# Optimization experiments

Hardware: AMD Instinct MI355X
Metric: run time of the kernel (lower is better)

The kernel has to match this reference:

```python
import jax, jax.numpy as jnp
import numpy as np

# irreps = 128x0e + 64x1o + 32x2e  ->  dim = 128 + 192 + 160 = 480
IRREPS = [(128, 0), (64, 1), (32, 2)]  # (multiplicity, l)
NUM_SCALAR = 128          # 0e channels (p=+1, l=0); scalar_index = [0..127]
NUM_FEATURES = 224        # total irrep instances
DIM = 480
EPS_LN = 1e-5             # unused by math path (kept for fidelity to signature)
EPS_INV = 1e-6            # Invariant eps (default)
N = 100000


def setup_inputs() -> dict:
    key = jax.random.key(0)
    k1, k2, k3 = jax.random.split(key, 3)
    node_input = jax.random.normal(k1, (N, DIM), dtype=jnp.float32)
    affine_weight = jax.random.normal(k2, (NUM_FEATURES,), dtype=jnp.float32)
    affine_bias = jax.random.normal(k3, (NUM_SCALAR,), dtype=jnp.float32)
    return {"node_input": node_input, "affine_weight": affine_weight, "affine_bias": affine_bias}


def _eln(x, weight, bias):
    # 1) subtract mean of scalar (0e) channels from those channels only
    scalar_mean = jnp.mean(x[:, :NUM_SCALAR], axis=1, keepdims=True)
    x = x.at[:, :NUM_SCALAR].add(-scalar_mean)

    # 2) per-irrep-instance norm: Invariant = Norm(x + eps^2) - eps
    norms = []
    off = 0
    for mul, l in IRREPS:
        d = 2 * l + 1
        blk = x[:, off: off + mul * d].reshape(x.shape[0], mul, d)
        n = jnp.sqrt(jnp.sum(jnp.square(blk + EPS_INV ** 2), axis=-1)) - EPS_INV
        norms.append(n)
        off += mul * d
    norm = jnp.concatenate(norms, axis=1)  # [N, num_features]

    # 3) RMS over irrep instances, scale whole feature vector
    inv_rms = jax.lax.rsqrt(jnp.mean(jnp.square(norm), axis=1, keepdims=True))
    x = x * inv_rms

    # 4) per-irrep affine scale (ElementwiseTensorProduct with num_features x 0e)
    w_parts = []
    ix = 0
    for mul, l in IRREPS:
        d = 2 * l + 1
        w_parts.append(jnp.repeat(weight[ix: ix + mul], d))
        ix += mul
    w_full = jnp.concatenate(w_parts)  # [dim]
    x = x * w_full[None, :]

    # 5) add bias to scalar channels
    x = x.at[:, :NUM_SCALAR].add(bias[None, :])
    return x


def reference(node_input, affine_weight, affine_bias):
    return _eln(node_input, affine_weight, affine_bias)
```

## Files before the change

kernel.cpp:

```cpp
#include <hip/hip_runtime.h>
#include <hip/hip_bf16.h>


#define NROW_TOTAL_DIM 480
#define ROWS_PER_BLOCK 4

__global__ __launch_bounds__(256) void eln_kernel(
    const float* __restrict__ in,
    const float* __restrict__ wgt,
    const float* __restrict__ bias,
    float* __restrict__ out,
    int n_rows)
{
    const int wave = threadIdx.x >> 6;
    const int lane = threadIdx.x & 63;
    const int row  = blockIdx.x * ROWS_PER_BLOCK + wave;
    if (row >= n_rows) return;

    const float* x = in  + (size_t)row * NROW_TOTAL_DIM;
    float*       y = out + (size_t)row * NROW_TOTAL_DIM;

    float2 s = *reinterpret_cast<const float2*>(x + 2 * lane);

    const float* p1 = x + 128 + 3 * lane;
    float v0 = p1[0], v1 = p1[1], v2 = p1[2];

    float e0 = 0.f, e1 = 0.f, e2 = 0.f, e3 = 0.f, e4 = 0.f;
    if (lane < 32) {
        const float* p2 = x + 320 + 5 * lane;
        e0 = p2[0]; e1 = p2[1]; e2 = p2[2]; e3 = p2[3]; e4 = p2[4];
    }

    float ssum = s.x + s.y;
    #pragma unroll
    for (int m = 1; m < 64; m <<= 1) ssum += __shfl_xor(ssum, m);
    const float mean = ssum * (1.0f / 128.0f);
    s.x -= mean;
    s.y -= mean;

    const float epsq = 1e-12f;
    const float eps  = 1e-6f;

    float n0 = fabsf(s.x + epsq) - eps;
    float n1 = fabsf(s.y + epsq) - eps;

    float a0 = v0 + epsq, a1 = v1 + epsq, a2 = v2 + epsq;
    float n2 = sqrtf(a0 * a0 + a1 * a1 + a2 * a2) - eps;

    float nsq = n0 * n0 + n1 * n1 + n2 * n2;

    if (lane < 32) {
        float b0 = e0 + epsq, b1 = e1 + epsq, b2 = e2 + epsq,
              b3 = e3 + epsq, b4 = e4 + epsq;
        float n3 = sqrtf(b0 * b0 + b1 * b1 + b2 * b2 + b3 * b3 + b4 * b4) - eps;
        nsq += n3 * n3;
    }

    #pragma unroll
    for (int m = 1; m < 64; m <<= 1) nsq += __shfl_xor(nsq, m);
    const float inv_rms = rsqrtf(nsq * (1.0f / 224.0f));

    {
        float w0 = wgt[2 * lane], w1 = wgt[2 * lane + 1];
        float2 so;
        so.x = s.x * inv_rms * w0 + bias[2 * lane];
        so.y = s.y * inv_rms * w1 + bias[2 * lane + 1];
        *reinterpret_cast<float2*>(y + 2 * lane) = so;
    }
    {
        float wv = wgt[128 + lane] * inv_rms;
        float* q1 = y + 128 + 3 * lane;
        q1[0] = v0 * wv;
        q1[1] = v1 * wv;
        q1[2] = v2 * wv;
    }
    if (lane < 32) {
        float we = wgt[192 + lane] * inv_rms;
        float* q2 = y + 320 + 5 * lane;
        q2[0] = e0 * we;
        q2[1] = e1 * we;
        q2[2] = e2 * we;
        q2[3] = e3 * we;
        q2[4] = e4 * we;
    }
}

extern "C" void kernel_launch(void* const* d_in, const int* in_sizes, int n_in,
                              void* d_out, int out_size, void* d_ws, size_t ws_size,
                              hipStream_t stream) {
    const float* node_input    = (const float*)d_in[0];
    const float* affine_weight = (const float*)d_in[1];
    const float* affine_bias   = (const float*)d_in[2];
    float* out = (float*)d_out;

    const int n_rows = in_sizes[0] / NROW_TOTAL_DIM;
    const int grid = (n_rows + ROWS_PER_BLOCK - 1) / ROWS_PER_BLOCK;

    eln_kernel<<<grid, 256, 0, stream>>>(node_input, affine_weight, affine_bias,
                                         out, n_rows);
}
```

Baseline: 72.32 us.

## Vectorize row loads to float4, hoist weights, use grid-stride persistent waves

Each wave now reads its 480-float row as contiguous 16-byte vectors with nontemporal loads and stores, replacing the strided 3- and 5-element per-lane accesses. Per-lane weight and bias values are loaded once into registers before a grid-stride loop over rows, and the grid is capped at 2048 blocks. The per-irrep norm-squared sum is replaced by a plain sum of squares over all elements, which removes the sqrt calls but drops the small -eps correction terms. Each wave keeps only one row in flight, so latency hiding depends on occupancy.

```diff
diff --git a/kernel.cpp b/kernel.cpp
--- a/kernel.cpp
+++ b/kernel.cpp
@@ -2,8 +2,9 @@
 #include <hip/hip_bf16.h>
 
 
-#define NROW_TOTAL_DIM 480
-#define ROWS_PER_BLOCK 4
+#define DIM 480
+
+typedef float f32x4 __attribute__((ext_vector_type(4)));
 
 __global__ __launch_bounds__(256) void eln_kernel(
     const float* __restrict__ in,
@@ -12,76 +13,69 @@
     float* __restrict__ out,
     int n_rows)
 {
-    const int wave = threadIdx.x >> 6;
-    const int lane = threadIdx.x & 63;
-    const int row  = blockIdx.x * ROWS_PER_BLOCK + wave;
-    if (row >= n_rows) return;
+    const int lane    = threadIdx.x & 63;
+    const int gwave   = (blockIdx.x * blockDim.x + threadIdx.x) >> 6;
+    const int n_waves = (gridDim.x * blockDim.x) >> 6;
 
-    const float* x = in  + (size_t)row * NROW_TOTAL_DIM;
-    float*       y = out + (size_t)row * NROW_TOTAL_DIM;
-
-    float2 s = *reinterpret_cast<const float2*>(x + 2 * lane);
-
-    const float* p1 = x + 128 + 3 * lane;
-    float v0 = p1[0], v1 = p1[1], v2 = p1[2];
-
-    float e0 = 0.f, e1 = 0.f, e2 = 0.f, e3 = 0.f, e4 = 0.f;
-    if (lane < 32) {
-        const float* p2 = x + 320 + 5 * lane;
-        e0 = p2[0]; e1 = p2[1]; e2 = p2[2]; e3 = p2[3]; e4 = p2[4];
+    float w0k[4], w1k[4], bk[4];
+    #pragma unroll
+    for (int k = 0; k < 4; ++k) {
+        int j = 4 * lane + k;
+        if (j < 128) { w0k[k] = wgt[j];                       bk[k] = bias[j]; }
+        else         { w0k[k] = wgt[128 + (j - 128) / 3];     bk[k] = 0.f;     }
+    }
+    #pragma unroll
+    for (int k = 0; k < 4; ++k) {
+        if (lane < 56) {
+            int j = 256 + 4 * lane + k;
+            w1k[k] = (j < 320) ? wgt[128 + (j - 128) / 3]
+                               : wgt[192 + (j - 320) / 5];
+        } else {
+            w1k[k] = 0.f;
+        }
     }
 
-    float ssum = s.x + s.y;
-    #pragma unroll
-    for (int m = 1; m < 64; m <<= 1) ssum += __shfl_xor(ssum, m);
-    const float mean = ssum * (1.0f / 128.0f);
-    s.x -= mean;
-    s.y -= mean;
+    const float epsq = 1e-12f;
 
-    const float epsq = 1e-12f;
-    const float eps  = 1e-6f;
+    for (int row = gwave; row < n_rows; row += n_waves) {
+        const f32x4* xr = reinterpret_cast<const f32x4*>(in + (size_t)row * DIM);
+        f32x4*       yr = reinterpret_cast<f32x4*>(out + (size_t)row * DIM);
 
-    float n0 = fabsf(s.x + epsq) - eps;
-    float n1 = fabsf(s.y + epsq) - eps;
+        f32x4 r0 = __builtin_nontemporal_load(xr + lane);
+        f32x4 r1 = (f32x4)(0.f);
+        if (lane < 56) r1 = __builtin_nontemporal_load(xr + 64 + lane);
 
-    float a0 = v0 + epsq, a1 = v1 + epsq, a2 = v2 + epsq;
-    float n2 = sqrtf(a0 * a0 + a1 * a1 + a2 * a2) - eps;
+        float ssum = (lane < 32) ? (r0.x + r0.y + r0.z + r0.w) : 0.f;
+        #pragma unroll
+        for (int m = 1; m < 64; m <<= 1) ssum += __shfl_xor(ssum, m);
+        const float mean = ssum * (1.0f / 128.0f);
+        if (lane < 32) { r0.x -= mean; r0.y -= mean; r0.z -= mean; r0.w -= mean; }
 
-    float nsq = n0 * n0 + n1 * n1 + n2 * n2;
+        float a0 = r0.x + epsq, a1 = r0.y + epsq, a2 = r0.z + epsq, a3 = r0.w + epsq;
+        float nsq = a0 * a0 + a1 * a1 + a2 * a2 + a3 * a3;
+        if (lane < 56) {
+            float c0 = r1.x + epsq, c1 = r1.y + epsq, c2 = r1.z + epsq, c3 = r1.w + epsq;
+            nsq += c0 * c0 + c1 * c1 + c2 * c2 + c3 * c3;
+        }
+        #pragma unroll
+        for (int m = 1; m < 64; m <<= 1) nsq += __shfl_xor(nsq, m);
+        const float inv_rms = rsqrtf(nsq * (1.0f / 224.0f));
 
-    if (lane < 32) {
-        float b0 = e0 + epsq, b1 = e1 + epsq, b2 = e2 + epsq,
-              b3 = e3 + epsq, b4 = e4 + epsq;
-        float n3 = sqrtf(b0 * b0 + b1 * b1 + b2 * b2 + b3 * b3 + b4 * b4) - eps;
-        nsq += n3 * n3;
-    }
+        f32x4 o0;
+        o0.x = r0.x * inv_rms * w0k[0] + bk[0];
+        o0.y = r0.y * inv_rms * w0k[1] + bk[1];
+        o0.z = r0.z * inv_rms * w0k[2] + bk[2];
+        o0.w = r0.w * inv_rms * w0k[3] + bk[3];
+        __builtin_nontemporal_store(o0, yr + lane);
 
-    #pragma unroll
-    for (int m = 1; m < 64; m <<= 1) nsq += __shfl_xor(nsq, m);
-    const float inv_rms = rsqrtf(nsq * (1.0f / 224.0f));
-
-    {
-        float w0 = wgt[2 * lane], w1 = wgt[2 * lane + 1];
-        float2 so;
-        so.x = s.x * inv_rms * w0 + bias[2 * lane];
-        so.y = s.y * inv_rms * w1 + bias[2 * lane + 1];
-        *reinterpret_cast<float2*>(y + 2 * lane) = so;
-    }
-    {
-        float wv = wgt[128 + lane] * inv_rms;
-        float* q1 = y + 128 + 3 * lane;
-        q1[0] = v0 * wv;
-        q1[1] = v1 * wv;
-        q1[2] = v2 * wv;
-    }
-    if (lane < 32) {
-        float we = wgt[192 + lane] * inv_rms;
-        float* q2 = y + 320 + 5 * lane;
-        q2[0] = e0 * we;
-        q2[1] = e1 * we;
-        q2[2] = e2 * we;
-        q2[3] = e3 * we;
-        q2[4] = e4 * we;
+        if (lane < 56) {
+            f32x4 o1;
+            o1.x = r1.x * inv_rms * w1k[0];
+            o1.y = r1.y * inv_rms * w1k[1];
+            o1.z = r1.z * inv_rms * w1k[2];
+            o1.w = r1.w * inv_rms * w1k[3];
+            __builtin_nontemporal_store(o1, yr + 64 + lane);
+        }
     }
 }
 
@@ -93,8 +87,9 @@
     const float* affine_bias   = (const float*)d_in[2];
     float* out = (float*)d_out;
 
-    const int n_rows = in_sizes[0] / NROW_TOTAL_DIM;
-    const int grid = (n_rows + ROWS_PER_BLOCK - 1) / ROWS_PER_BLOCK;
+    const int n_rows = in_sizes[0] / DIM;
+    int grid = (n_rows + 3) / 4;
+    if (grid > 2048) grid = 2048;
 
     eln_kernel<<<grid, 256, 0, stream>>>(node_input, affine_weight, affine_bias,
                                          out, n_rows);
```

Result: no change. 72.78 us (+0.6%).
